# Optimization experiments

Measured on AMD Instinct MI355X. Metric: run time of the kernel, lower is better.

Reference implementation:

```python
import jax, jax.numpy as jnp
import numpy as np

B, S1, S2 = 16, 256, 512          # batch, vision len, text len
V_HID, T_HID = 1024, 768          # v_hidden_size, hidden_size
BI_HID, H = 1024, 8               # bi_hidden_size, bi_num_attention_heads
D = BI_HID // H                   # attention_head_size = 128


def setup_inputs() -> dict:
    key = jax.random.key(0)
    ks = jax.random.split(key, 16)
    s = 0.02
    inp = {
        "input_tensor1": jax.random.normal(ks[0], (B, S1, V_HID), jnp.float32),
        "attention_mask1": jnp.zeros((B, 1, 1, S1), jnp.float32),
        "input_tensor2": jax.random.normal(ks[1], (B, S2, T_HID), jnp.float32),
        "attention_mask2": jnp.zeros((B, 1, 1, S2), jnp.float32),
        # vision-stream projections (query1/key1/value1): v_hidden -> all_head_size
        "Wq1": jax.random.normal(ks[2], (V_HID, BI_HID), jnp.float32) * s,
        "bq1": jnp.zeros((BI_HID,), jnp.float32),
        "Wk1": jax.random.normal(ks[3], (V_HID, BI_HID), jnp.float32) * s,
        "bk1": jnp.zeros((BI_HID,), jnp.float32),
        "Wv1": jax.random.normal(ks[4], (V_HID, BI_HID), jnp.float32) * s,
        "bv1": jnp.zeros((BI_HID,), jnp.float32),
        # text-stream projections (query2/key2/value2): hidden -> all_head_size
        "Wq2": jax.random.normal(ks[5], (T_HID, BI_HID), jnp.float32) * s,
        "bq2": jnp.zeros((BI_HID,), jnp.float32),
        "Wk2": jax.random.normal(ks[6], (T_HID, BI_HID), jnp.float32) * s,
        "bk2": jnp.zeros((BI_HID,), jnp.float32),
        "Wv2": jax.random.normal(ks[7], (T_HID, BI_HID), jnp.float32) * s,
        "bv2": jnp.zeros((BI_HID,), jnp.float32),
    }
    return inp


def _heads(x):
    # [B, S, H*D] -> [B, S, H, D]
    b, s, _ = x.shape
    return x.reshape(b, s, H, D)


def reference(input_tensor1, attention_mask1, input_tensor2, attention_mask2,
              Wq1, bq1, Wk1, bk1, Wv1, bv1,
              Wq2, bq2, Wk2, bk2, Wv2, bv2):
    scale = 1.0 / jnp.sqrt(jnp.asarray(D, input_tensor1.dtype))
    # stream 1 (vision) QKV
    q1 = _heads(input_tensor1 @ Wq1 + bq1)
    k1 = _heads(input_tensor1 @ Wk1 + bk1)
    v1 = _heads(input_tensor1 @ Wv1 + bv1)
    # stream 2 (text) QKV
    q2 = _heads(input_tensor2 @ Wq2 + bq2)
    k2 = _heads(input_tensor2 @ Wk2 + bk2)
    v2 = _heads(input_tensor2 @ Wv2 + bv2)

    # attention 1: text queries attend to vision keys/values  -> context1 [B,S2,BI_HID]
    scores1 = jnp.einsum('bqhd,bkhd->bhqk', q2, k1) * scale + attention_mask1
    probs1 = jax.nn.softmax(scores1, axis=-1)  # dropout prob = 0 (eval)
    context1 = jnp.einsum('bhqk,bkhd->bqhd', probs1, v1).reshape(B, S2, BI_HID)

    # attention 2: vision queries attend to text keys/values  -> context2 [B,S1,BI_HID]
    scores2 = jnp.einsum('bqhd,bkhd->bhqk', q1, k2) * scale + attention_mask2
    probs2 = jax.nn.softmax(scores2, axis=-1)
    context2 = jnp.einsum('bhqk,bkhd->bqhd', probs2, v2).reshape(B, S1, BI_HID)

    return (context1, context2)
```

## Files before the change

### kernel.cpp

```cpp
#include <hip/hip_runtime.h>


typedef _Float16 f16;
typedef unsigned int u32;
typedef f16  v8h __attribute__((ext_vector_type(8)));
typedef float v4f __attribute__((ext_vector_type(4)));

struct alignas(8) h4 { f16 x, y, z, w; };

#define GLL16(g, l) __builtin_amdgcn_global_load_lds(                          \
    (const __attribute__((address_space(1))) u32*)(g),                         \
    (__attribute__((address_space(3))) u32*)(l), 16, 0, 0)

#define MFMA16 __builtin_amdgcn_mfma_f32_16x16x32_f16

__global__ __launch_bounds__(256)
void cvt_in(const float* __restrict__ p1, long n1,
            const float* __restrict__ p2, long n2,
            f16* __restrict__ d1, f16* __restrict__ d2)
{
    long i = ((long)blockIdx.x * 256 + threadIdx.x) * 8;
    const float* s; f16* d;
    if (i < n1) { s = p1 + i; d = d1 + i; }
    else        { long j = i - n1; if (j >= n2) return; s = p2 + j; d = d2 + j; }
    float4 a = *(const float4*)s, b = *(const float4*)(s + 4);
    v8h o = {(f16)a.x, (f16)a.y, (f16)a.z, (f16)a.w,
             (f16)b.x, (f16)b.y, (f16)b.z, (f16)b.w};
    *(v8h*)d = o;
}

__global__ __launch_bounds__(256)
void cvt_wT(const float* __restrict__ w0, const float* __restrict__ w1,
            const float* __restrict__ w2, const float* __restrict__ w3,
            const float* __restrict__ w4, const float* __restrict__ w5,
            f16* __restrict__ o1, f16* __restrict__ o2)
{
    const int z = blockIdx.z;
    const int K = z < 3 ? 1024 : 768;
    const int bk = blockIdx.y * 64;
    if (bk >= K) return;
    const float* src = z == 0 ? w0 : z == 1 ? w1 : z == 2 ? w2
                     : z == 3 ? w3 : z == 4 ? w4 : w5;
    f16* dst = z < 3 ? o1 + (size_t)z * 1024 * 1024
                     : o2 + (size_t)(z - 3) * 1024 * 768;

    __shared__ float t[64][65];
    const int bn = blockIdx.x * 64;
    const int r0 = threadIdx.x >> 4, c4 = (threadIdx.x & 15) * 4;
#pragma unroll
    for (int rr = 0; rr < 64; rr += 16) {
        float4 v = *(const float4*)&src[(long)(bk + rr + r0) * 1024 + bn + c4];
        t[rr + r0][c4 + 0] = v.x; t[rr + r0][c4 + 1] = v.y;
        t[rr + r0][c4 + 2] = v.z; t[rr + r0][c4 + 3] = v.w;
    }
    __syncthreads();
#pragma unroll
    for (int rr = 0; rr < 64; rr += 16) {
        const int n = rr + r0;
        h4 o = {(f16)t[c4 + 0][n], (f16)t[c4 + 1][n],
                (f16)t[c4 + 2][n], (f16)t[c4 + 3][n]};
        *(h4*)&dst[(long)(bn + n) * K + bk + c4] = o;
    }
}

__global__ __launch_bounds__(256, 4)
void mm_proj(const f16* __restrict__ A2, const f16* __restrict__ B2,
             const float* __restrict__ bq2, const float* __restrict__ bk2,
             const float* __restrict__ bv2,
             f16* __restrict__ q2o, f16* __restrict__ k2o, f16* __restrict__ v2o,
             const f16* __restrict__ A1, const f16* __restrict__ B1,
             const float* __restrict__ bq1, const float* __restrict__ bk1,
             const float* __restrict__ bv1,
             f16* __restrict__ q1o, f16* __restrict__ k1o, f16* __restrict__ v1o)
{
    __shared__ f16 sh[16384];

    const int gid = blockIdx.x;
    const bool is2 = gid < 1536;
    const int id   = is2 ? gid : gid - 1536;
    const int K    = is2 ? 768 : 1024;
    const int S    = is2 ? 512 : 256;
    const int mdiv = is2 ? 8 : 4;
    const f16* A  = is2 ? A2 : A1;
    const f16* Bw = is2 ? B2 : B1;

    const int by = (id & 7) * mdiv + ((id >> 3) % mdiv);
    const int bx = id / (8 * mdiv);
    const int m0 = by * 128, n0 = bx * 128;

    const int tid = threadIdx.x, lane = tid & 63, w = tid >> 6;
    const int wm = w >> 1, wn = w & 1;
    const int fr = lane & 15, fq = lane >> 4;

    int aoff[4], boff[4];
#pragma unroll
    for (int t = 0; t < 4; ++t) {
        const int ra = wm * 64 + t * 16 + fr;
        aoff[t] = ra * 32 + (fq ^ (ra & 3)) * 8;
        const int rb = wn * 64 + t * 16 + fr;
        boff[t] = rb * 32 + (fq ^ (rb & 3)) * 8;
    }

    auto stage = [&](int k0, int p) {
        f16* Ad = sh + p * 4096;
        f16* Bd = sh + 8192 + p * 4096;
#pragma unroll
        for (int j = 0; j < 2; ++j) {
            const int c = j * 256 + tid, row = c >> 2;
            const int kl = (c & 3) ^ (row & 3);
            GLL16(A  + (long)(m0 + row) * K + k0 + kl * 8, Ad + c * 8);
            GLL16(Bw + (long)(n0 + row) * K + k0 + kl * 8, Bd + c * 8);
        }
    };

    v4f acc[4][4];
#pragma unroll
    for (int i = 0; i < 4; ++i)
#pragma unroll
        for (int j = 0; j < 4; ++j) acc[i][j] = (v4f){0.f, 0.f, 0.f, 0.f};

    stage(0, 0);
    const int NK = K >> 5;
    for (int kt = 0; kt < NK; ++kt) {
        __syncthreads();
        if (kt + 1 < NK) stage((kt + 1) << 5, (kt + 1) & 1);
        const f16* As = sh + (kt & 1) * 4096;
        const f16* Bs = sh + 8192 + (kt & 1) * 4096;
        v8h ah[4], bh[4];
#pragma unroll
        for (int t = 0; t < 4; ++t) ah[t] = *(const v8h*)&As[aoff[t]];
#pragma unroll
        for (int t = 0; t < 4; ++t) bh[t] = *(const v8h*)&Bs[boff[t]];
#pragma unroll
        for (int tmi = 0; tmi < 4; ++tmi)
#pragma unroll
            for (int tni = 0; tni < 4; ++tni)
                acc[tmi][tni] = MFMA16(ah[tmi], bh[tni], acc[tmi][tni], 0, 0, 0);
    }

    const int col = lane & 15, quad = lane >> 4;
    const int seg = n0 >> 10, nbase = n0 & 1023;
    f16* buf = sh;

    if (seg < 2) {
        const float* bias = seg == 0 ? (is2 ? bq2 : bq1) : (is2 ? bk2 : bk1);
        f16* Co = seg == 0 ? (is2 ? q2o : q1o) : (is2 ? k2o : k1o);
#pragma unroll
        for (int pass = 0; pass < 2; ++pass) {
            __syncthreads();
            if (wm == pass) {
#pragma unroll
                for (int tmi = 0; tmi < 4; ++tmi) {
                    const int ml = tmi * 16 + quad * 4;
#pragma unroll
                    for (int tni = 0; tni < 4; ++tni) {
                        const int nl = wn * 64 + tni * 16 + col;
                        const float bvl = bias[nbase + nl];
#pragma unroll
                        for (int i = 0; i < 4; ++i)
                            buf[(ml + i) * 136 + nl] = (f16)(acc[tmi][tni][i] + bvl);
                    }
                }
            }
            __syncthreads();
            const int rr = tid >> 2, cc = (tid & 3) * 32;
            const long gb = (long)(m0 + pass * 64 + rr) * 1024 + nbase + cc;
#pragma unroll
            for (int c = 0; c < 4; ++c)
                *(v8h*)&Co[gb + c * 8] = *(const v8h*)&buf[rr * 136 + cc + c * 8];
        }
    } else {
        const float* bias = is2 ? bv2 : bv1;
        f16* vo = is2 ? v2o : v1o;
        const int bb = m0 / S, s0 = m0 % S;
#pragma unroll
        for (int pass = 0; pass < 2; ++pass) {
            __syncthreads();
            if (wn == pass) {
#pragma unroll
                for (int tmi = 0; tmi < 4; ++tmi) {
                    const int ml = wm * 64 + tmi * 16 + quad * 4;
#pragma unroll
                    for (int tni = 0; tni < 4; ++tni) {
                        const int nl = tni * 16 + col;
                        const float bvl = bias[nbase + pass * 64 + nl];
                        h4 o = {(f16)(acc[tmi][tni][0] + bvl),
                                (f16)(acc[tmi][tni][1] + bvl),
                                (f16)(acc[tmi][tni][2] + bvl),
                                (f16)(acc[tmi][tni][3] + bvl)};
                        *(h4*)&buf[nl * 136 + ml] = o;
                    }
                }
            }
            __syncthreads();
            const int nn = tid >> 2, mm = (tid & 3) * 32;
            const long gb = ((long)bb * 1024 + nbase + pass * 64 + nn) * S + s0 + mm;
#pragma unroll
            for (int c = 0; c < 4; ++c)
                *(v8h*)&vo[gb + c * 8] = *(const v8h*)&buf[nn * 136 + mm + c * 8];
        }
    }
}

__global__ __launch_bounds__(256, 3)
void flash(const f16* __restrict__ q2, const f16* __restrict__ k1,
           const f16* __restrict__ v1, const float* __restrict__ m1,
           float* __restrict__ o1,
           const f16* __restrict__ q1, const f16* __restrict__ k2,
           const f16* __restrict__ v2, const float* __restrict__ m2,
           float* __restrict__ o2, float scale)
{
    constexpr int PSTR = 72;
    __shared__ f16 lds[16384 + 64 * PSTR];
    f16* KL = lds;
    f16* VL = lds + 8192;
    f16* PL = lds + 16384;
    f16* QL = lds;

    const int gid = blockIdx.x;
    const bool ph1 = gid < 1024;
    const int id = ph1 ? gid : gid - 1024;
    const int Sq = ph1 ? 512 : 256, Sk = ph1 ? 256 : 512;
    const f16* qp = ph1 ? q2 : q1;
    const f16* kp = ph1 ? k1 : k2;
    const f16* vp = ph1 ? v1 : v2;
    const float* mask = ph1 ? m1 : m2;
    float* out = ph1 ? o1 : o2;

    const int zz = id & 127, yy = id >> 7;
    const int b = zz >> 3, hd = zz & 7;
    const int q0 = yy * 64;
    const int tid = threadIdx.x, lane = tid & 63, w = tid >> 6;
    const int col = lane & 15, quad = lane >> 4;

    const long qoff = ((long)b * Sq + q0) * 1024 + (long)hd * 128;
#pragma unroll
    for (int j = 0; j < 4; ++j) {
        const int c = j * 256 + tid, row = c >> 4, ch = (c & 15) ^ (row & 15);
        GLL16(qp + qoff + (long)row * 1024 + ch * 8, QL + c * 8);
    }
    __syncthreads();
    v8h qf[4];
    {
        const int row = w * 16 + col;
#pragma unroll
        for (int kf = 0; kf < 4; ++kf)
            qf[kf] = *(const v8h*)&QL[row * 128 + ((kf * 4 + quad) ^ (row & 15)) * 8];
    }

    v8h ones;
#pragma unroll
    for (int i = 0; i < 8; ++i) ones[i] = (f16)1.0f;

    v4f O[8], Lc;
#pragma unroll
    for (int nj = 0; nj < 8; ++nj) O[nj] = (v4f){0.f, 0.f, 0.f, 0.f};
    Lc = (v4f){0.f, 0.f, 0.f, 0.f};

    const long kbase = (long)b * Sk * 1024 + (long)hd * 128;
    const long vbase = ((long)b * 1024 + hd * 128) * (long)Sk;

    for (int kt = 0; kt < (Sk >> 6); ++kt) {
        __syncthreads();
#pragma unroll
        for (int j = 0; j < 4; ++j) {
            const int c = j * 256 + tid, row = c >> 4, ch = (c & 15) ^ (row & 15);
            GLL16(kp + kbase + (long)(kt * 64 + row) * 1024 + ch * 8, KL + c * 8);
        }
#pragma unroll
        for (int j = 0; j < 4; ++j) {
            const int c = j * 256 + tid, row = c >> 3, ch = (c & 7) ^ (row & 7);
            GLL16(vp + vbase + (long)row * Sk + kt * 64 + ch * 8, VL + c * 8);
        }
        __syncthreads();

        v4f sa[4];
#pragma unroll
        for (int tn = 0; tn < 4; ++tn) sa[tn] = (v4f){0.f, 0.f, 0.f, 0.f};
#pragma unroll
        for (int kf = 0; kf < 4; ++kf) {
            v8h bh[4];
#pragma unroll
            for (int tn = 0; tn < 4; ++tn) {
                const int row = tn * 16 + col;
                bh[tn] = *(const v8h*)&KL[row * 128 + ((kf * 4 + quad) ^ (row & 15)) * 8];
            }
#pragma unroll
            for (int tn = 0; tn < 4; ++tn)
                sa[tn] = MFMA16(qf[kf], bh[tn], sa[tn], 0, 0, 0);
        }

        float mv[4];
#pragma unroll
        for (int tn = 0; tn < 4; ++tn)
            mv[tn] = mask[(long)b * Sk + kt * 64 + tn * 16 + col];
#pragma unroll
        for (int tn = 0; tn < 4; ++tn)
#pragma unroll
            for (int r = 0; r < 4; ++r) {
                const float p = __expf(sa[tn][r] * scale + mv[tn]);
                PL[(w * 16 + quad * 4 + r) * PSTR + tn * 16 + col] = (f16)p;
            }

#pragma unroll
        for (int kf2 = 0; kf2 < 2; ++kf2) {
            v8h vb[8];
#pragma unroll
            for (int nj = 0; nj < 8; ++nj) {
                const int row = nj * 16 + col;
                vb[nj] = *(const v8h*)&VL[row * 64 + ((kf2 * 4 + quad) ^ (row & 7)) * 8];
            }
            const v8h pa = *(const v8h*)&PL[(w * 16 + col) * PSTR + kf2 * 32 + quad * 8];
#pragma unroll
            for (int nj = 0; nj < 8; ++nj)
                O[nj] = MFMA16(pa, vb[nj], O[nj], 0, 0, 0);
            Lc = MFMA16(pa, ones, Lc, 0, 0, 0);
        }
    }

    float inv[4];
#pragma unroll
    for (int r = 0; r < 4; ++r) inv[r] = 1.0f / Lc[r];
    const long ob = ((long)b * Sq + q0 + w * 16 + quad * 4) * 1024 + (long)hd * 128;
#pragma unroll
    for (int nj = 0; nj < 8; ++nj)
#pragma unroll
        for (int r = 0; r < 4; ++r)
            out[ob + (long)r * 1024 + nj * 16 + col] = O[nj][r] * inv[r];
}

extern "C" void kernel_launch(void* const* d_in, const int* in_sizes, int n_in,
                              void* d_out, int out_size, void* d_ws, size_t ws_size,
                              hipStream_t stream)
{
    const float* in1   = (const float*)d_in[0];
    const float* mask1 = (const float*)d_in[1];
    const float* in2   = (const float*)d_in[2];
    const float* mask2 = (const float*)d_in[3];
    const float* Wq1 = (const float*)d_in[4];  const float* bq1 = (const float*)d_in[5];
    const float* Wk1 = (const float*)d_in[6];  const float* bk1 = (const float*)d_in[7];
    const float* Wv1 = (const float*)d_in[8];  const float* bv1 = (const float*)d_in[9];
    const float* Wq2 = (const float*)d_in[10]; const float* bq2 = (const float*)d_in[11];
    const float* Wk2 = (const float*)d_in[12]; const float* bk2 = (const float*)d_in[13];
    const float* Wv2 = (const float*)d_in[14]; const float* bv2 = (const float*)d_in[15];

    constexpr int Bb = 16, S1 = 256, S2 = 512, VH = 1024, TH = 768;
    constexpr long M1 = (long)Bb * S1, M2 = (long)Bb * S2;
    const float scale = 0.088388347648318447f;

    f16* W = (f16*)d_ws;
    f16* i1  = W;
    f16* i2  = i1 + M1 * VH;
    f16* w1  = i2 + M2 * TH;
    f16* w2  = w1 + (long)3072 * VH;
    f16* q1  = w2 + (long)3072 * TH;
    f16* k1  = q1 + M1 * 1024;
    f16* v1t = k1 + M1 * 1024;
    f16* q2  = v1t + M1 * 1024;
    f16* k2  = q2 + M2 * 1024;
    f16* v2t = k2 + M2 * 1024;
    float* out = (float*)d_out;

    cvt_in<<<dim3(5120), 256, 0, stream>>>(in1, M1 * VH, in2, M2 * TH, i1, i2);
    cvt_wT<<<dim3(16, 16, 6), 256, 0, stream>>>(Wq1, Wk1, Wv1, Wq2, Wk2, Wv2, w1, w2);

    mm_proj<<<dim3(2304), 256, 0, stream>>>(
        i2, w2, bq2, bk2, bv2, q2, k2, v2t,
        i1, w1, bq1, bk1, bv1, q1, k1, v1t);

    flash<<<dim3(1536), 256, 0, stream>>>(
        q2, k1, v1t, mask1, out,
        q1, k2, v2t, mask2, out + M2 * 1024, scale);
}
```

Measured before the change: 262.4 us.

## Double flash query tile per block, reorder phases, change GEMM LDS swizzle

```diff
diff --git a/kernel.cpp b/kernel.cpp
--- a/kernel.cpp
+++ b/kernel.cpp
@@ -96,9 +96,9 @@
 #pragma unroll
     for (int t = 0; t < 4; ++t) {
         const int ra = wm * 64 + t * 16 + fr;
-        aoff[t] = ra * 32 + (fq ^ (ra & 3)) * 8;
+        aoff[t] = ra * 32 + (fq ^ ((ra >> 1) & 3)) * 8;
         const int rb = wn * 64 + t * 16 + fr;
-        boff[t] = rb * 32 + (fq ^ (rb & 3)) * 8;
+        boff[t] = rb * 32 + (fq ^ ((rb >> 1) & 3)) * 8;
     }
 
     auto stage = [&](int k0, int p) {
@@ -107,7 +107,7 @@
 #pragma unroll
         for (int j = 0; j < 2; ++j) {
             const int c = j * 256 + tid, row = c >> 2;
-            const int kl = (c & 3) ^ (row & 3);
+            const int kl = (c & 3) ^ ((row >> 1) & 3);
             GLL16(A  + (long)(m0 + row) * K + k0 + kl * 8, Ad + c * 8);
             GLL16(Bw + (long)(n0 + row) * K + k0 + kl * 8, Bd + c * 8);
         }
@@ -202,7 +202,7 @@
     }
 }
 
-__global__ __launch_bounds__(256, 3)
+__global__ __launch_bounds__(256, 2)
 void flash(const f16* __restrict__ q2, const f16* __restrict__ k1,
            const f16* __restrict__ v1, const float* __restrict__ m1,
            float* __restrict__ o1,
@@ -211,56 +211,59 @@
            float* __restrict__ o2, float scale)
 {
     constexpr int PSTR = 72;
-    __shared__ f16 lds[16384 + 64 * PSTR];
+    __shared__ f16 lds[16384 + 128 * PSTR];
     f16* KL = lds;
     f16* VL = lds + 8192;
     f16* PL = lds + 16384;
-    f16* QL = lds;
 
     const int gid = blockIdx.x;
-    const bool ph1 = gid < 1024;
-    const int id = ph1 ? gid : gid - 1024;
-    const int Sq = ph1 ? 512 : 256, Sk = ph1 ? 256 : 512;
-    const f16* qp = ph1 ? q2 : q1;
-    const f16* kp = ph1 ? k1 : k2;
-    const f16* vp = ph1 ? v1 : v2;
-    const float* mask = ph1 ? m1 : m2;
-    float* out = ph1 ? o1 : o2;
+    const bool ph2 = gid < 256;
+    const int id = ph2 ? gid : gid - 256;
+    const int Sq = ph2 ? 256 : 512, Sk = ph2 ? 512 : 256;
+    const f16* qp = ph2 ? q1 : q2;
+    const f16* kp = ph2 ? k2 : k1;
+    const f16* vp = ph2 ? v2 : v1;
+    const float* mask = ph2 ? m2 : m1;
+    float* out = ph2 ? o2 : o1;
 
     const int zz = id & 127, yy = id >> 7;
     const int b = zz >> 3, hd = zz & 7;
-    const int q0 = yy * 64;
+    const int q0 = yy * 128;
     const int tid = threadIdx.x, lane = tid & 63, w = tid >> 6;
     const int col = lane & 15, quad = lane >> 4;
 
-    const long qoff = ((long)b * Sq + q0) * 1024 + (long)hd * 128;
-#pragma unroll
-    for (int j = 0; j < 4; ++j) {
-        const int c = j * 256 + tid, row = c >> 4, ch = (c & 15) ^ (row & 15);
-        GLL16(qp + qoff + (long)row * 1024 + ch * 8, QL + c * 8);
-    }
-    __syncthreads();
-    v8h qf[4];
-    {
-        const int row = w * 16 + col;
+    v8h qf[2][4];
+#pragma unroll
+    for (int rt = 0; rt < 2; ++rt) {
+        const long qr = ((long)b * Sq + q0 + w * 32 + rt * 16 + col) * 1024
+                        + (long)hd * 128;
 #pragma unroll
         for (int kf = 0; kf < 4; ++kf)
-            qf[kf] = *(const v8h*)&QL[row * 128 + ((kf * 4 + quad) ^ (row & 15)) * 8];
+            qf[rt][kf] = *(const v8h*)(qp + qr + kf * 32 + quad * 8);
     }
 
     v8h ones;
 #pragma unroll
     for (int i = 0; i < 8; ++i) ones[i] = (f16)1.0f;
 
-    v4f O[8], Lc;
-#pragma unroll
-    for (int nj = 0; nj < 8; ++nj) O[nj] = (v4f){0.f, 0.f, 0.f, 0.f};
-    Lc = (v4f){0.f, 0.f, 0.f, 0.f};
+    v4f O[2][8], Lc[2];
+#pragma unroll
+    for (int rt = 0; rt < 2; ++rt) {
+#pragma unroll
+        for (int nj = 0; nj < 8; ++nj) O[rt][nj] = (v4f){0.f, 0.f, 0.f, 0.f};
+        Lc[rt] = (v4f){0.f, 0.f, 0.f, 0.f};
+    }
 
     const long kbase = (long)b * Sk * 1024 + (long)hd * 128;
     const long vbase = ((long)b * 1024 + hd * 128) * (long)Sk;
-
-    for (int kt = 0; kt < (Sk >> 6); ++kt) {
+    const int nk = Sk >> 6;
+
+    float mv[4];
+#pragma unroll
+    for (int tn = 0; tn < 4; ++tn)
+        mv[tn] = mask[(long)b * Sk + tn * 16 + col];
+
+    for (int kt = 0; kt < nk; ++kt) {
         __syncthreads();
 #pragma unroll
         for (int j = 0; j < 4; ++j) {
@@ -272,11 +275,19 @@
             const int c = j * 256 + tid, row = c >> 3, ch = (c & 7) ^ (row & 7);
             GLL16(vp + vbase + (long)row * Sk + kt * 64 + ch * 8, VL + c * 8);
         }
+        float mvn[4];
+        if (kt + 1 < nk) {
+#pragma unroll
+            for (int tn = 0; tn < 4; ++tn)
+                mvn[tn] = mask[(long)b * Sk + (kt + 1) * 64 + tn * 16 + col];
+        }
         __syncthreads();
 
-        v4f sa[4];
-#pragma unroll
-        for (int tn = 0; tn < 4; ++tn) sa[tn] = (v4f){0.f, 0.f, 0.f, 0.f};
+        v4f sa[2][4];
+#pragma unroll
+        for (int rt = 0; rt < 2; ++rt)
+#pragma unroll
+            for (int tn = 0; tn < 4; ++tn) sa[rt][tn] = (v4f){0.f, 0.f, 0.f, 0.f};
 #pragma unroll
         for (int kf = 0; kf < 4; ++kf) {
             v8h bh[4];
@@ -286,21 +297,22 @@
                 bh[tn] = *(const v8h*)&KL[row * 128 + ((kf * 4 + quad) ^ (row & 15)) * 8];
             }
 #pragma unroll
+            for (int rt = 0; rt < 2; ++rt)
+#pragma unroll
+                for (int tn = 0; tn < 4; ++tn)
+                    sa[rt][tn] = MFMA16(qf[rt][kf], bh[tn], sa[rt][tn], 0, 0, 0);
+        }
+
+#pragma unroll
+        for (int rt = 0; rt < 2; ++rt)
+#pragma unroll
             for (int tn = 0; tn < 4; ++tn)
-                sa[tn] = MFMA16(qf[kf], bh[tn], sa[tn], 0, 0, 0);
-        }
-
-        float mv[4];
-#pragma unroll
-        for (int tn = 0; tn < 4; ++tn)
-            mv[tn] = mask[(long)b * Sk + kt * 64 + tn * 16 + col];
-#pragma unroll
-        for (int tn = 0; tn < 4; ++tn)
-#pragma unroll
-            for (int r = 0; r < 4; ++r) {
-                const float p = __expf(sa[tn][r] * scale + mv[tn]);
-                PL[(w * 16 + quad * 4 + r) * PSTR + tn * 16 + col] = (f16)p;
-            }
+#pragma unroll
+                for (int r = 0; r < 4; ++r) {
+                    const float p = __expf(sa[rt][tn][r] * scale + mv[tn]);
+                    PL[(w * 32 + rt * 16 + quad * 4 + r) * PSTR + tn * 16 + col]
+                        = (f16)p;
+                }
 
 #pragma unroll
         for (int kf2 = 0; kf2 < 2; ++kf2) {
@@ -310,23 +322,33 @@
                 const int row = nj * 16 + col;
                 vb[nj] = *(const v8h*)&VL[row * 64 + ((kf2 * 4 + quad) ^ (row & 7)) * 8];
             }
-            const v8h pa = *(const v8h*)&PL[(w * 16 + col) * PSTR + kf2 * 32 + quad * 8];
-#pragma unroll
-            for (int nj = 0; nj < 8; ++nj)
-                O[nj] = MFMA16(pa, vb[nj], O[nj], 0, 0, 0);
-            Lc = MFMA16(pa, ones, Lc, 0, 0, 0);
-        }
-    }
-
-    float inv[4];
-#pragma unroll
-    for (int r = 0; r < 4; ++r) inv[r] = 1.0f / Lc[r];
-    const long ob = ((long)b * Sq + q0 + w * 16 + quad * 4) * 1024 + (long)hd * 128;
-#pragma unroll
-    for (int nj = 0; nj < 8; ++nj)
-#pragma unroll
-        for (int r = 0; r < 4; ++r)
-            out[ob + (long)r * 1024 + nj * 16 + col] = O[nj][r] * inv[r];
+#pragma unroll
+            for (int rt = 0; rt < 2; ++rt) {
+                const v8h pa = *(const v8h*)&PL[(w * 32 + rt * 16 + col) * PSTR
+                                                + kf2 * 32 + quad * 8];
+#pragma unroll
+                for (int nj = 0; nj < 8; ++nj)
+                    O[rt][nj] = MFMA16(pa, vb[nj], O[rt][nj], 0, 0, 0);
+                Lc[rt] = MFMA16(pa, ones, Lc[rt], 0, 0, 0);
+            }
+        }
+#pragma unroll
+        for (int tn = 0; tn < 4; ++tn) mv[tn] = mvn[tn];
+    }
+
+#pragma unroll
+    for (int rt = 0; rt < 2; ++rt) {
+        float inv[4];
+#pragma unroll
+        for (int r = 0; r < 4; ++r) inv[r] = 1.0f / Lc[rt][r];
+        const long ob = ((long)b * Sq + q0 + w * 32 + rt * 16 + quad * 4) * 1024
+                        + (long)hd * 128;
+#pragma unroll
+        for (int nj = 0; nj < 8; ++nj)
+#pragma unroll
+            for (int r = 0; r < 4; ++r)
+                out[ob + (long)r * 1024 + nj * 16 + col] = O[rt][nj][r] * inv[r];
+    }
 }
 
 extern "C" void kernel_launch(void* const* d_in, const int* in_sizes, int n_in,
@@ -368,7 +390,7 @@
         i2, w2, bq2, bk2, bv2, q2, k2, v2t,
         i1, w1, bq1, bk1, bv1, q1, k1, v1t);
 
-    flash<<<dim3(1536), 256, 0, stream>>>(
+    flash<<<dim3(768), 256, 0, stream>>>(
         q2, k1, v1t, mask1, out,
         q1, k2, v2t, mask2, out + M2 * 1024, scale);
 }
```

Result: faster. 255.4 us (-2.7%).
